# Optimization experiments

Measured on AMD Instinct MI355X. Metric: run time of the kernel, lower is better.

Reference implementation:

```python
import jax, jax.numpy as jnp
import numpy as np

B, S, D, H, F, E = 2, 1024, 1024, 16, 2048, 8
HD = D // H


def _ln(x, g, b, eps=1e-5):
    m = x.mean(-1, keepdims=True)
    v = ((x - m) ** 2).mean(-1, keepdims=True)
    return (x - m) / jnp.sqrt(v + eps) * g + b


def setup_inputs() -> dict:
    key = jax.random.key(0)
    ks = jax.random.split(key, 12)
    rn = lambda k, shp, s=0.02: jax.random.normal(k, shp, jnp.float32) * s
    return {
        'src': jax.random.normal(ks[0], (B, S, D), jnp.float32),
        'q_w': rn(ks[1], (D, D)),
        'k_w': rn(ks[2], (D, D)),
        'v_w': rn(ks[3], (D, D)),
        'out_w': rn(ks[4], (D, D)),
        'gate_w': rn(ks[5], (D, D)),
        'gate_b': rn(ks[6], (D,)),
        'scale_w': rn(ks[7], (H, HD)),
        'n1_g': jnp.ones((D,), jnp.float32),
        'n1_b': jnp.zeros((D,), jnp.float32),
        'n2_g': jnp.ones((D,), jnp.float32),
        'n2_b': jnp.zeros((D,), jnp.float32),
        'moe_gate_w': rn(ks[8], (D, E)),
        'moe_gate_b': jnp.zeros((E,), jnp.float32),
        'w1': rn(ks[9], (E, D, F)),
        'b1': jnp.zeros((E, F), jnp.float32),
        'ln_g': jnp.ones((E, F), jnp.float32),
        'ln_b': jnp.zeros((E, F), jnp.float32),
        'w2': rn(ks[10], (E, F, D)),
        'b2': jnp.zeros((E, D), jnp.float32),
        'res_scale': jnp.ones((E,), jnp.float32),
    }


def reference(src, q_w, k_w, v_w, out_w, gate_w, gate_b, scale_w,
              n1_g, n1_b, n2_g, n2_b, moe_gate_w, moe_gate_b,
              w1, b1, ln_g, ln_b, w2, b2, res_scale):
    b, s, d = src.shape
    h = scale_w.shape[0]
    hd = d // h
    # --- MemoAttention (gated, dynamically scaled), eval mode ---
    q = (src @ q_w).reshape(b, s, h, hd).transpose(0, 2, 1, 3)  # [b,h,s,hd]
    k = (src @ k_w).reshape(b, s, h, hd).transpose(0, 2, 1, 3)
    v = (src @ v_w).reshape(b, s, h, hd).transpose(0, 2, 1, 3)
    scores = jnp.einsum('bhqd,bhkd->bhqk', q, k) / np.float32(np.sqrt(hd))
    scale = jax.nn.sigmoid(jnp.einsum('bhsd,hd->bhs', q, scale_w)) * 2.0
    scores = scores * scale[..., None]
    aw = jax.nn.softmax(scores, axis=-1)
    out = jnp.einsum('bhqk,bhkd->bhqd', aw, v).transpose(0, 2, 1, 3).reshape(b, s, d)
    gate = jax.nn.sigmoid(out @ gate_w + gate_b)
    attn = (out * gate) @ out_w
    # --- residual + norm1 ---
    x = _ln(src + attn, n1_g, n1_b)
    # --- MoE FFN (top-2 routing; torch loop overwrites -> last (max-index) expert
    xr = x.reshape(-1, d)                      # [N, d]
    n = xr.shape[0]
    logits = xr @ moe_gate_w + moe_gate_b       # [N, E]
    top_v, top_i = jax.lax.top_k(logits, 2)
    wts = jax.nn.softmax(top_v, axis=-1)        # [N, 2]
    chosen = jnp.max(top_i, axis=-1)            # last-written expert per token

    def expert(W1, B1, G, Bt, W2, B2, rsc):
        hh = xr @ W1 + B1                       # [N, F]
        hh = jax.nn.gelu(_ln(hh, G, Bt), approximate=False)
        return (hh @ W2 + B2) * rsc + xr        # [N, d]

    outs = jax.vmap(expert)(w1, b1, ln_g, ln_b, w2, b2, res_scale)  # [E,N,d]
    sel = jnp.take_along_axis(outs.transpose(1, 0, 2), chosen[:, None, None], axis=1)[:, 0]
    moe = sel * jnp.sum(wts, axis=-1, keepdims=True)
    # --- residual + norm2 ---
    return _ln(x + moe.reshape(b, s, d), n2_g, n2_b)
```

## Files before the change

### kernel.cpp

```cpp
#include <hip/hip_runtime.h>


typedef _Float16 f16;
typedef _Float16 f16x8 __attribute__((ext_vector_type(8)));
typedef _Float16 f16x4 __attribute__((ext_vector_type(4)));
typedef float f32x4 __attribute__((ext_vector_type(4)));

constexpr int CS  = 1024;
constexpr int CD  = 1024;
constexpr int CH  = 16;
constexpr int CHD = 64;
constexpr int CF  = 2048;
constexpr int CE  = 8;
constexpr int CN  = 2048;
constexpr int CBH = 32;
constexpr int KS  = 512;
constexpr int MAXT = 24;

constexpr float LO_SCALE = 2048.f;
constexpr float LO_INV   = 1.f / 2048.f;

#define MFMA16(a, b, c) __builtin_amdgcn_mfma_f32_16x16x32_f16((a), (b), (c), 0, 0, 0)

#define TO_GBL(p) ((const __attribute__((address_space(1))) void*)(p))
#define TO_LDS(p) ((__attribute__((address_space(3))) void*)(p))
#define GLD16(g, l) __builtin_amdgcn_global_load_lds(TO_GBL(g), TO_LDS(l), 16, 0, 0)

__device__ __forceinline__ void fsplit(float v, f16 &hi, f16 &lo) {
  hi = (f16)v;
  lo = (f16)((v - (float)hi) * LO_SCALE);
}


__global__ void k_split_cvt(const float* __restrict__ in, f16* __restrict__ oh,
                            f16* __restrict__ ol, int n) {
  int i = (blockIdx.x * blockDim.x + threadIdx.x) * 4;
  if (i >= n) return;
  float4 v = *(const float4*)(in + i);
  float a[4] = {v.x, v.y, v.z, v.w};
  f16x4 vh, vl;
#pragma unroll
  for (int j = 0; j < 4; ++j) {
    f16 hi = (f16)a[j];
    vh[j] = hi;
    vl[j] = (f16)((a[j] - (float)hi) * LO_SCALE);
  }
  *(f16x4*)(oh + i) = vh;
  *(f16x4*)(ol + i) = vl;
}

__global__ __launch_bounds__(256) void k_transpose_split(
    const float* __restrict__ in, f16* __restrict__ oh,
    f16* __restrict__ ol, int R, int C) {
  __shared__ float t[64][65];
  const int z = blockIdx.z;
  const float* src = in + (size_t)z * R * C;
  f16* dh = oh + (size_t)z * R * C;
  f16* dl = ol ? ol + (size_t)z * R * C : nullptr;
  const int c0 = blockIdx.x * 64, r0 = blockIdx.y * 64;
  const int tt = threadIdx.x;
  const int lane = tt & 63, wv = tt >> 6;
#pragma unroll
  for (int i = 0; i < 16; ++i)
    t[wv + i * 4][lane] = src[(size_t)(r0 + wv + i * 4) * C + c0 + lane];
  __syncthreads();
  const int oc = tt >> 4;
  const int og = tt & 15;
#pragma unroll
  for (int cc = 0; cc < 64; cc += 16) {
    f16x4 vh, vl;
#pragma unroll
    for (int j = 0; j < 4; ++j) {
      const float v = t[og * 4 + j][cc + oc];
      f16 hi = (f16)v;
      vh[j] = hi;
      vl[j] = (f16)((v - (float)hi) * LO_SCALE);
    }
    const size_t idx = (size_t)(c0 + cc + oc) * R + r0 + og * 4;
    *(f16x4*)(dh + idx) = vh;
    if (dl) *(f16x4*)(dl + idx) = vl;
  }
}


template <bool SPLIT>
__device__ __forceinline__ void gemm_tile128(
    const f16* a0, const f16* a1, const f16* al0, const f16* al1,
    const f16* b0, const f16* b1, const f16* bl0, const f16* bl1,
    int K, f16* lds, f32x4 (&accm)[4][4], f32x4 (&accc)[4][4]) {
  constexpr int BUF = SPLIT ? 16384 : 8192;
  constexpr int BO  = SPLIT ? 8192 : 4096;
  const int t = threadIdx.x;
  const int lane = t & 63, wave = t >> 6;
  const int wm = wave >> 1, wn = wave & 1;
  const int m16 = lane & 15, quad = lane >> 4;
  int aoff[4], boff[4];
#pragma unroll
  for (int s = 0; s < 4; ++s) {
    const int ra = wm * 64 + s * 16 + m16;
    aoff[s] = ra * 32 + ((quad ^ ((ra >> 1) & 3)) * 8);
    const int rb = wn * 64 + s * 16 + m16;
    boff[s] = BO + rb * 32 + ((quad ^ ((rb >> 1) & 3)) * 8);
  }
  auto stage = [&](f16* buf) {
    GLD16(a0, buf + t * 8);
    GLD16(a1, buf + 2048 + t * 8);
    GLD16(b0, buf + BO + t * 8);
    GLD16(b1, buf + BO + 2048 + t * 8);
    if constexpr (SPLIT) {
      GLD16(al0, buf + 4096 + t * 8);
      GLD16(al1, buf + 6144 + t * 8);
      GLD16(bl0, buf + 12288 + t * 8);
      GLD16(bl1, buf + 14336 + t * 8);
      al0 += 32; al1 += 32; bl0 += 32; bl1 += 32;
    }
    a0 += 32; a1 += 32; b0 += 32; b1 += 32;
  };
  stage(lds);
  int cur = 0;
  for (int k = 0; k < K; k += 32) {
    __syncthreads();
    f16* buf = lds + cur * BUF;
    if (k + 32 < K) stage(lds + (cur ^ 1) * BUF);
    f16x8 af[4], alf[4];
#pragma unroll
    for (int s = 0; s < 4; ++s) {
      af[s] = *(const f16x8*)(buf + aoff[s]);
      if constexpr (SPLIT) alf[s] = *(const f16x8*)(buf + 4096 + aoff[s]);
    }
#pragma unroll
    for (int sn = 0; sn < 4; ++sn) {
      const f16x8 bf = *(const f16x8*)(buf + boff[sn]);
#pragma unroll
      for (int sm = 0; sm < 4; ++sm)
        accm[sm][sn] = MFMA16(af[sm], bf, accm[sm][sn]);
      if constexpr (SPLIT) {
        const f16x8 blf = *(const f16x8*)(buf + 4096 + boff[sn]);
#pragma unroll
        for (int sm = 0; sm < 4; ++sm)
          accc[sm][sn] = MFMA16(af[sm], blf, accc[sm][sn]);
#pragma unroll
        for (int sm = 0; sm < 4; ++sm)
          accc[sm][sn] = MFMA16(alf[sm], bf, accc[sm][sn]);
      }
    }
    cur ^= 1;
  }
}


__global__ __launch_bounds__(256, 2) void g_qkv(
    const f16* __restrict__ srcH, const f16* __restrict__ srcL,
    const f16* __restrict__ qwH, const f16* __restrict__ qwL,
    const f16* __restrict__ kwH, const f16* __restrict__ kwL,
    const f16* __restrict__ vwH, const f16* __restrict__ vwL,
    f16* __restrict__ qHo, f16* __restrict__ qLo,
    f16* __restrict__ kHo, f16* __restrict__ kLo,
    f16* __restrict__ vTH, f16* __restrict__ vTL) {
  __shared__ f16 lds[32768];
  const int z = blockIdx.z;
  const int m0 = blockIdx.x * 128, n0 = blockIdx.y * 128;
  const int t = threadIdx.x;
  const int rowS = t >> 2;
  const int ksw = ((t & 3) ^ ((rowS >> 1) & 3)) * 8;
  const f16* BH = (z == 0) ? qwH : (z == 1) ? kwH : vwH;
  const f16* BL = (z == 0) ? qwL : (z == 1) ? kwL : vwL;
  const f16* A0 = srcH + (size_t)(m0 + rowS) * CD + ksw;
  const f16* AL0 = srcL + (size_t)(m0 + rowS) * CD + ksw;
  const f16* B0 = BH + (size_t)(n0 + rowS) * CD + ksw;
  const f16* BL0 = BL + (size_t)(n0 + rowS) * CD + ksw;
  const f32x4 VZ = {0.f, 0.f, 0.f, 0.f};
  f32x4 accm[4][4], accc[4][4];
#pragma unroll
  for (int i = 0; i < 4; ++i)
#pragma unroll
    for (int j = 0; j < 4; ++j) { accm[i][j] = VZ; accc[i][j] = VZ; }
  gemm_tile128<true>(A0, A0 + (size_t)64 * CD, AL0, AL0 + (size_t)64 * CD,
                     B0, B0 + (size_t)64 * CD, BL0, BL0 + (size_t)64 * CD,
                     CD, lds, accm, accc);
  const int lane = t & 63, wave = t >> 6;
  const int wm = wave >> 1, wn = wave & 1;
  const int m16 = lane & 15, quad = lane >> 4;
#pragma unroll
  for (int sm = 0; sm < 4; ++sm)
#pragma unroll
    for (int sn = 0; sn < 4; ++sn)
#pragma unroll
      for (int r = 0; r < 4; ++r) {
        const int row = m0 + wm * 64 + sm * 16 + quad * 4 + r;
        const int col = n0 + wn * 64 + sn * 16 + m16;
        const float v = accm[sm][sn][r] + accc[sm][sn][r] * LO_INV;
        f16 hi, lo; fsplit(v, hi, lo);
        const int bb = row >> 10, ss = row & 1023;
        const int hh = col >> 6, hd = col & 63;
        if (z == 2) {
          const size_t idx = ((size_t)((bb * CH + hh) * CHD + hd)) * CS + ss;
          vTH[idx] = hi; vTL[idx] = lo;
        } else {
          const size_t idx = ((size_t)((bb * CH + hh) * CS + ss)) * CHD + hd;
          if (z == 0) { qHo[idx] = hi; qLo[idx] = lo; }
          else        { kHo[idx] = hi; kLo[idx] = lo; }
        }
      }
}


__device__ __forceinline__ int pswz(int q, int k) {
  return q * 64 + ((((k >> 2) ^ q) & 15) << 2) + (k & 3);
}

__global__ __launch_bounds__(256) void k_fattn(
    const f16* __restrict__ qH_, const f16* __restrict__ qL_,
    const f16* __restrict__ kH_, const f16* __restrict__ kL_,
    const f16* __restrict__ vTH_, const f16* __restrict__ vTL_,
    const float* __restrict__ scale_w,
    f16* __restrict__ aoH, f16* __restrict__ aoL) {
  __shared__ f16 kvb[32768];
  __shared__ float psc[4 * 1024];
  const int bh = blockIdx.y;
  const int b = bh >> 4, h = bh & 15;
  const int t = threadIdx.x;
  const int lane = t & 63, wave = t >> 6;
  const int m16 = lane & 15, quad = lane >> 4;
  const int q0 = blockIdx.x * 64 + wave * 16;
  float* P = psc + wave * 1024;
  const f32x4 VZ = {0.f, 0.f, 0.f, 0.f};
  const size_t kb = (size_t)bh * CS * CHD;

  const int rowS = t >> 3, chS = t & 7;
  auto stage = [&](f16* dst, int kc) {
#pragma unroll
    for (int i = 0; i < 2; ++i) {
      const int row = rowS + 32 * i;
      const int sc = (chS ^ (row & 7)) * 8;
      GLD16(kH_ + kb + (size_t)(kc + row) * CHD + sc, dst + i * 2048 + t * 8);
      GLD16(kL_ + kb + (size_t)(kc + row) * CHD + sc, dst + 4096 + i * 2048 + t * 8);
      GLD16(vTH_ + kb + (size_t)row * CS + kc + sc, dst + 8192 + i * 2048 + t * 8);
      GLD16(vTL_ + kb + (size_t)row * CS + kc + sc, dst + 12288 + i * 2048 + t * 8);
    }
  };
  auto ldf = [&](const f16* piece, int r, int q) -> f16x8 {
    return *(const f16x8*)(piece + r * 64 + ((q ^ (r & 7)) * 8));
  };

  const f16* qrh = qH_ + ((size_t)bh * CS + q0 + m16) * CHD + quad * 8;
  const f16* qrl = qL_ + ((size_t)bh * CS + q0 + m16) * CHD + quad * 8;
  f16x8 a0h = *(const f16x8*)(qrh);
  f16x8 a1h = *(const f16x8*)(qrh + 32);
  f16x8 a0l = *(const f16x8*)(qrl);
  f16x8 a1l = *(const f16x8*)(qrl + 32);

  stage(kvb, 0);

  float dot = 0.f;
  {
    const float* sw = scale_w + h * CHD + quad * 8;
    float4 s0 = *(const float4*)(sw);
    float4 s1 = *(const float4*)(sw + 4);
    float4 s2 = *(const float4*)(sw + 32);
    float4 s3 = *(const float4*)(sw + 36);
    float sv[16] = {s0.x, s0.y, s0.z, s0.w, s1.x, s1.y, s1.z, s1.w,
                    s2.x, s2.y, s2.z, s2.w, s3.x, s3.y, s3.z, s3.w};
#pragma unroll
    for (int j = 0; j < 8; ++j) {
      dot += ((float)a0h[j] + (float)a0l[j] * LO_INV) * sv[j];
      dot += ((float)a1h[j] + (float)a1l[j] * LO_INV) * sv[8 + j];
    }
    dot += __shfl_xor(dot, 16);
    dot += __shfl_xor(dot, 32);
  }
  const float qsv = 2.f / (1.f + __expf(-dot));
  float qsr[4];
#pragma unroll
  for (int r = 0; r < 4; ++r) qsr[r] = __shfl(qsv, quad * 4 + r) * 0.125f;

  f32x4 accm[4], accc[4], accd[4];
#pragma unroll
  for (int tt = 0; tt < 4; ++tt) { accm[tt] = VZ; accc[tt] = VZ; accd[tt] = VZ; }
  float mrun[4], lrun[4];
#pragma unroll
  for (int r = 0; r < 4; ++r) { mrun[r] = -1e30f; lrun[r] = 0.f; }

  int cur = 0;
  for (int kc = 0; kc < CS; kc += 64) {
    __syncthreads();
    const f16* kv = kvb + cur * 16384;
    if (kc + 64 < CS) stage(kvb + (cur ^ 1) * 16384, kc + 64);

    f32x4 st[4];
#pragma unroll
    for (int tt = 0; tt < 4; ++tt) {
      const int r = tt * 16 + m16;
      f16x8 b0h = ldf(kv,        r, quad);
      f16x8 b1h = ldf(kv,        r, quad + 4);
      f16x8 b0l = ldf(kv + 4096, r, quad);
      f16x8 b1l = ldf(kv + 4096, r, quad + 4);
      f32x4 am = VZ, ac1 = VZ, ac2 = VZ;
      am = MFMA16(a0h, b0h, am); am = MFMA16(a1h, b1h, am);
      ac1 = MFMA16(a0h, b0l, ac1); ac2 = MFMA16(a0l, b0h, ac2);
      ac1 = MFMA16(a1h, b1l, ac1); ac2 = MFMA16(a1l, b1h, ac2);
#pragma unroll
      for (int r4 = 0; r4 < 4; ++r4)
        st[tt][r4] = (am[r4] + (ac1[r4] + ac2[r4]) * LO_INV) * qsr[r4];
    }
    float alpha[4];
#pragma unroll
    for (int r = 0; r < 4; ++r) {
      float mx = fmaxf(fmaxf(st[0][r], st[1][r]), fmaxf(st[2][r], st[3][r]));
#pragma unroll
      for (int msk = 8; msk >= 1; msk >>= 1) mx = fmaxf(mx, __shfl_xor(mx, msk));
      const float mnew = fmaxf(mrun[r], mx);
      alpha[r] = __expf(mrun[r] - mnew);
      mrun[r] = mnew;
    }
    float rs[4] = {0.f, 0.f, 0.f, 0.f};
#pragma unroll
    for (int tt = 0; tt < 4; ++tt)
#pragma unroll
      for (int r = 0; r < 4; ++r) {
        const float e = __expf(st[tt][r] - mrun[r]);
        rs[r] += e;
        P[pswz(quad * 4 + r, tt * 16 + m16)] = e;
      }
#pragma unroll
    for (int r = 0; r < 4; ++r) {
#pragma unroll
      for (int msk = 8; msk >= 1; msk >>= 1) rs[r] += __shfl_xor(rs[r], msk);
      lrun[r] = lrun[r] * alpha[r] + rs[r];
#pragma unroll
      for (int tt = 0; tt < 4; ++tt) {
        accm[tt][r] *= alpha[r]; accc[tt][r] *= alpha[r]; accd[tt][r] *= alpha[r];
      }
    }
    f16x8 pah[2], pal[2];
#pragma unroll
    for (int c = 0; c < 2; ++c) {
      const int k0 = c * 32 + quad * 8;
      float4 p0 = *(const float4*)(P + pswz(m16, k0));
      float4 p1 = *(const float4*)(P + pswz(m16, k0 + 4));
      float pv[8] = {p0.x, p0.y, p0.z, p0.w, p1.x, p1.y, p1.z, p1.w};
#pragma unroll
      for (int j = 0; j < 8; ++j) {
        f16 hi = (f16)pv[j];
        pah[c][j] = hi;
        pal[c][j] = (f16)((pv[j] - (float)hi) * LO_SCALE);
      }
    }
#pragma unroll
    for (int c = 0; c < 2; ++c)
#pragma unroll
      for (int tt = 0; tt < 4; ++tt) {
        const int r = tt * 16 + m16;
        f16x8 vbh = ldf(kv + 8192,  r, quad + 4 * c);
        f16x8 vbl = ldf(kv + 12288, r, quad + 4 * c);
        accm[tt] = MFMA16(pah[c], vbh, accm[tt]);
        accc[tt] = MFMA16(pah[c], vbl, accc[tt]);
        accd[tt] = MFMA16(pal[c], vbh, accd[tt]);
      }
    cur ^= 1;
  }
#pragma unroll
  for (int tt = 0; tt < 4; ++tt)
#pragma unroll
    for (int r = 0; r < 4; ++r) {
      const int row = q0 + quad * 4 + r;
      const float v =
          (accm[tt][r] + (accc[tt][r] + accd[tt][r]) * LO_INV) / lrun[r];
      f16 hi, lo; fsplit(v, hi, lo);
      const size_t idx = ((size_t)(b * CS + row)) * CD + h * CHD + tt * 16 + m16;
      aoH[idx] = hi; aoL[idx] = lo;
    }
}


__global__ __launch_bounds__(256, 2) void g_gate(
    const f16* __restrict__ aoH, const f16* __restrict__ aoL,
    const f16* __restrict__ gwH, const f16* __restrict__ gwL,
    float* __restrict__ gpre ) {
  __shared__ f16 lds[32768];
  const int m0 = blockIdx.x * 128, n0 = blockIdx.y * 128, s = blockIdx.z;
  const int t = threadIdx.x;
  const int rowS = t >> 2;
  const int ksw = ((t & 3) ^ ((rowS >> 1) & 3)) * 8;
  const int k0 = s * KS;
  const f16* A0 = aoH + (size_t)(m0 + rowS) * CD + k0 + ksw;
  const f16* AL0 = aoL + (size_t)(m0 + rowS) * CD + k0 + ksw;
  const f16* B0 = gwH + (size_t)(n0 + rowS) * CD + k0 + ksw;
  const f16* BL0 = gwL + (size_t)(n0 + rowS) * CD + k0 + ksw;
  const f32x4 VZ = {0.f, 0.f, 0.f, 0.f};
  f32x4 accm[4][4], accc[4][4];
#pragma unroll
  for (int i = 0; i < 4; ++i)
#pragma unroll
    for (int j = 0; j < 4; ++j) { accm[i][j] = VZ; accc[i][j] = VZ; }
  gemm_tile128<true>(A0, A0 + (size_t)64 * CD, AL0, AL0 + (size_t)64 * CD,
                     B0, B0 + (size_t)64 * CD, BL0, BL0 + (size_t)64 * CD,
                     KS, lds, accm, accc);
  float* gp = gpre + (size_t)s * CN * CD;
  const int lane = t & 63, wave = t >> 6;
  const int wm = wave >> 1, wn = wave & 1;
  const int m16 = lane & 15, quad = lane >> 4;
#pragma unroll
  for (int sm = 0; sm < 4; ++sm)
#pragma unroll
    for (int sn = 0; sn < 4; ++sn)
#pragma unroll
      for (int r = 0; r < 4; ++r) {
        const int row = m0 + wm * 64 + sm * 16 + quad * 4 + r;
        const int col = n0 + wn * 64 + sn * 16 + m16;
        gp[(size_t)row * CD + col] = accm[sm][sn][r] + accc[sm][sn][r] * LO_INV;
      }
}

__global__ __launch_bounds__(256) void k_gatemul(
    const float* __restrict__ gpre, const f16* __restrict__ aoH,
    const f16* __restrict__ aoL, const float* __restrict__ gate_b,
    f16* __restrict__ gdH, f16* __restrict__ gdL) {
  const int i = (blockIdx.x * 256 + threadIdx.x) * 4;
  float4 p0 = *(const float4*)(gpre + i);
  float4 p1 = *(const float4*)(gpre + (size_t)CN * CD + i);
  float4 gb = *(const float4*)(gate_b + (i & (CD - 1)));
  f16x4 ah = *(const f16x4*)(aoH + i);
  f16x4 al = *(const f16x4*)(aoL + i);
  float pre[4] = {p0.x + p1.x + gb.x, p0.y + p1.y + gb.y,
                  p0.z + p1.z + gb.z, p0.w + p1.w + gb.w};
  f16x4 oh, ol;
#pragma unroll
  for (int j = 0; j < 4; ++j) {
    const float g = 1.f / (1.f + __expf(-pre[j]));
    const float ov = ((float)ah[j] + (float)al[j] * LO_INV) * g;
    f16 hi, lo; fsplit(ov, hi, lo);
    oh[j] = hi; ol[j] = lo;
  }
  *(f16x4*)(gdH + i) = oh;
  *(f16x4*)(gdL + i) = ol;
}

__global__ __launch_bounds__(256, 2) void g_outp(
    const f16* __restrict__ gdH, const f16* __restrict__ gdL,
    const f16* __restrict__ owH, const f16* __restrict__ owL,
    float* __restrict__ y1p ) {
  __shared__ f16 lds[32768];
  const int m0 = blockIdx.x * 128, n0 = blockIdx.y * 128, s = blockIdx.z;
  const int t = threadIdx.x;
  const int rowS = t >> 2;
  const int ksw = ((t & 3) ^ ((rowS >> 1) & 3)) * 8;
  const int k0 = s * KS;
  const f16* A0 = gdH + (size_t)(m0 + rowS) * CD + k0 + ksw;
  const f16* AL0 = gdL + (size_t)(m0 + rowS) * CD + k0 + ksw;
  const f16* B0 = owH + (size_t)(n0 + rowS) * CD + k0 + ksw;
  const f16* BL0 = owL + (size_t)(n0 + rowS) * CD + k0 + ksw;
  const f32x4 VZ = {0.f, 0.f, 0.f, 0.f};
  f32x4 accm[4][4], accc[4][4];
#pragma unroll
  for (int i = 0; i < 4; ++i)
#pragma unroll
    for (int j = 0; j < 4; ++j) { accm[i][j] = VZ; accc[i][j] = VZ; }
  gemm_tile128<true>(A0, A0 + (size_t)64 * CD, AL0, AL0 + (size_t)64 * CD,
                     B0, B0 + (size_t)64 * CD, BL0, BL0 + (size_t)64 * CD,
                     KS, lds, accm, accc);
  float* yp = y1p + (size_t)s * CN * CD;
  const int lane = t & 63, wave = t >> 6;
  const int wm = wave >> 1, wn = wave & 1;
  const int m16 = lane & 15, quad = lane >> 4;
#pragma unroll
  for (int sm = 0; sm < 4; ++sm)
#pragma unroll
    for (int sn = 0; sn < 4; ++sn)
#pragma unroll
      for (int r = 0; r < 4; ++r) {
        const int row = m0 + wm * 64 + sm * 16 + quad * 4 + r;
        const int col = n0 + wn * 64 + sn * 16 + m16;
        yp[(size_t)row * CD + col] = accm[sm][sn][r] + accc[sm][sn][r] * LO_INV;
      }
}


__device__ __forceinline__ void block_reduce2(float &s, float &ss, float* red) {
#pragma unroll
  for (int msk = 32; msk >= 1; msk >>= 1) {
    s += __shfl_xor(s, msk);
    ss += __shfl_xor(ss, msk);
  }
  const int wave = threadIdx.x >> 6, lane = threadIdx.x & 63;
  if (lane == 0) { red[wave] = s; red[4 + wave] = ss; }
  __syncthreads();
  s = red[0] + red[1] + red[2] + red[3];
  ss = red[4] + red[5] + red[6] + red[7];
}

__global__ __launch_bounds__(256) void k_ln1(
    const float* __restrict__ y1p, const float* __restrict__ srcp,
    const float* __restrict__ g, const float* __restrict__ bb,
    float* __restrict__ x, f16* __restrict__ xH) {
  __shared__ float red[8];
  const int n = blockIdx.x;
  const int t = threadIdx.x;
  const size_t off = (size_t)n * CD + t * 4;
  float4 v0 = *(const float4*)(y1p + off);
  float4 v1 = *(const float4*)(y1p + (size_t)CN * CD + off);
  float4 v2 = *(const float4*)(srcp + off);
  float a[4] = {v0.x + v1.x + v2.x, v0.y + v1.y + v2.y,
                v0.z + v1.z + v2.z, v0.w + v1.w + v2.w};
  float s = a[0] + a[1] + a[2] + a[3];
  float ss = a[0]*a[0] + a[1]*a[1] + a[2]*a[2] + a[3]*a[3];
  block_reduce2(s, ss, red);
  const float mean = s * (1.f / CD);
  const float var = ss * (1.f / CD) - mean * mean;
  const float rstd = rsqrtf(var + 1e-5f);
#pragma unroll
  for (int j = 0; j < 4; ++j) {
    const int d = t * 4 + j;
    const float val = (a[j] - mean) * rstd * g[d] + bb[d];
    x[(size_t)n * CD + d] = val;
    xH[(size_t)n * CD + d] = (f16)val;
  }
}

__global__ __launch_bounds__(256) void k_ln2(
    const float* __restrict__ zbp, const float* __restrict__ x,
    const float* __restrict__ b2, const float* __restrict__ rsc,
    const int* __restrict__ chosen,
    const float* __restrict__ g, const float* __restrict__ bb,
    float* __restrict__ outp) {
  __shared__ float red[8];
  const int n = blockIdx.x;
  const int e = chosen[n];
  const float rs = rsc[e];
  const int t = threadIdx.x;
  const size_t off = (size_t)n * CD + t * 4;
  float4 p0 = *(const float4*)(zbp + off);
  float4 p1 = *(const float4*)(zbp + (size_t)CN * CD + off);
  float4 p2 = *(const float4*)(zbp + (size_t)2 * CN * CD + off);
  float4 p3 = *(const float4*)(zbp + (size_t)3 * CN * CD + off);
  float4 xv = *(const float4*)(x + off);
  float4 bv = *(const float4*)(b2 + (size_t)e * CD + t * 4);
  float a[4] = {2.f * xv.x + (p0.x + p1.x + p2.x + p3.x + bv.x) * rs,
                2.f * xv.y + (p0.y + p1.y + p2.y + p3.y + bv.y) * rs,
                2.f * xv.z + (p0.z + p1.z + p2.z + p3.z + bv.z) * rs,
                2.f * xv.w + (p0.w + p1.w + p2.w + p3.w + bv.w) * rs};
  float s = a[0] + a[1] + a[2] + a[3];
  float ss = a[0]*a[0] + a[1]*a[1] + a[2]*a[2] + a[3]*a[3];
  block_reduce2(s, ss, red);
  const float mean = s * (1.f / CD);
  const float var = ss * (1.f / CD) - mean * mean;
  const float rstd = rsqrtf(var + 1e-5f);
#pragma unroll
  for (int j = 0; j < 4; ++j) {
    const int d = t * 4 + j;
    outp[(size_t)n * CD + d] = (a[j] - mean) * rstd * g[d] + bb[d];
  }
}


__global__ void k_zero_counts(int* counts) {
  if (threadIdx.x < CE) counts[threadIdx.x] = 0;
}

__global__ __launch_bounds__(256) void k_route(
    const float* __restrict__ x, const float* __restrict__ gw, const float* __restrict__ gb,
    int* __restrict__ chosen, int* __restrict__ counts, int* __restrict__ bucket) {
  const int wave = threadIdx.x >> 6, lane = threadIdx.x & 63;
  const int n = blockIdx.x * 4 + wave;
  const float* xr = x + (size_t)n * CD;
  float acc[CE];
#pragma unroll
  for (int e = 0; e < CE; ++e) acc[e] = 0.f;
  for (int j = 0; j < 16; ++j) {
    const int d = lane * 16 + j;
    const float xv = xr[d];
    const float* wr = gw + (size_t)d * CE;
#pragma unroll
    for (int e = 0; e < CE; ++e) acc[e] += xv * wr[e];
  }
#pragma unroll
  for (int msk = 32; msk >= 1; msk >>= 1) {
#pragma unroll
    for (int e = 0; e < CE; ++e) acc[e] += __shfl_xor(acc[e], msk);
  }
  if (lane == 0) {
    float best = -1e30f, second = -1e30f;
    int bi = 0, si = 0;
#pragma unroll
    for (int e = 0; e < CE; ++e) {
      const float L = acc[e] + gb[e];
      if (L > best) { second = best; si = bi; best = L; bi = e; }
      else if (L > second) { second = L; si = e; }
    }
    const int ch = bi > si ? bi : si;
    chosen[n] = ch;
    const int pos = atomicAdd(&counts[ch], 1);
    bucket[ch * CN + pos] = n;
  }
}

__global__ void k_plan(const int* __restrict__ counts, int* __restrict__ tiles) {
  if (threadIdx.x == 0) {
    int n = 0;
    for (int e = 0; e < CE; ++e) {
      const int c = counts[e];
      for (int m0 = 0; m0 < c; m0 += 128) { tiles[2 * n] = e; tiles[2 * n + 1] = m0; ++n; }
    }
    for (; n < MAXT; ++n) { tiles[2 * n] = -1; tiles[2 * n + 1] = 0; }
  }
}


__global__ __launch_bounds__(256, 2) void g_moe1(
    const f16* __restrict__ xH, const f16* __restrict__ w1t,
    const int* __restrict__ counts, const int* __restrict__ bucket,
    const int* __restrict__ tiles, float* __restrict__ hbp ) {
  const int e = tiles[2 * blockIdx.x];
  if (e < 0) return;
  const int m0 = tiles[2 * blockIdx.x + 1];
  const int cnt = counts[e];
  const int s = blockIdx.z;
  __shared__ f16 lds[16384];
  const int t = threadIdx.x;
  const int rowS = t >> 2;
  const int ksw = ((t & 3) ^ ((rowS >> 1) & 3)) * 8;
  const int k0 = s * KS;
  int ra0 = m0 + rowS;      if (ra0 > cnt - 1) ra0 = cnt - 1;
  int ra1 = m0 + rowS + 64; if (ra1 > cnt - 1) ra1 = cnt - 1;
  const int tok0 = bucket[e * CN + ra0];
  const int tok1 = bucket[e * CN + ra1];
  const int n0 = blockIdx.y * 128;
  const f16* B0 = w1t + ((size_t)e * CF + n0 + rowS) * CD + k0 + ksw;
  const f32x4 VZ = {0.f, 0.f, 0.f, 0.f};
  f32x4 accm[4][4], accd[4][4];
#pragma unroll
  for (int i = 0; i < 4; ++i)
#pragma unroll
    for (int j = 0; j < 4; ++j) { accm[i][j] = VZ; accd[i][j] = VZ; }
  gemm_tile128<false>(xH + (size_t)tok0 * CD + k0 + ksw,
                      xH + (size_t)tok1 * CD + k0 + ksw, nullptr, nullptr,
                      B0, B0 + (size_t)64 * CD, nullptr, nullptr,
                      KS, lds, accm, accd);
  float* hp = hbp + (size_t)s * CN * CF;
  const int lane = t & 63, wave = t >> 6;
  const int wm = wave >> 1, wn = wave & 1;
  const int m16 = lane & 15, quad = lane >> 4;
#pragma unroll
  for (int sm = 0; sm < 4; ++sm)
#pragma unroll
    for (int sn = 0; sn < 4; ++sn)
#pragma unroll
      for (int r = 0; r < 4; ++r) {
        const int rr = m0 + wm * 64 + sm * 16 + quad * 4 + r;
        if (rr >= cnt) continue;
        const int tok = bucket[e * CN + rr];
        const int col = n0 + wn * 64 + sn * 16 + m16;
        hp[(size_t)tok * CF + col] = accm[sm][sn][r];
      }
}

__global__ __launch_bounds__(256) void k_lngelu(
    const float* __restrict__ hbp, const int* __restrict__ chosen,
    const float* __restrict__ b1,
    const float* __restrict__ ln_g, const float* __restrict__ ln_b,
    f16* __restrict__ h2) {
  __shared__ float red[8];
  const int n = blockIdx.x;
  const int e = chosen[n];
  const int t = threadIdx.x;
  const size_t off = (size_t)n * CF + t * 8;
  float4 v0 = *(const float4*)(hbp + off);
  float4 v1 = *(const float4*)(hbp + off + 4);
  float4 u0 = *(const float4*)(hbp + (size_t)CN * CF + off);
  float4 u1 = *(const float4*)(hbp + (size_t)CN * CF + off + 4);
  float4 b0 = *(const float4*)(b1 + (size_t)e * CF + t * 8);
  float4 b1v = *(const float4*)(b1 + (size_t)e * CF + t * 8 + 4);
  float a[8] = {v0.x + u0.x + b0.x, v0.y + u0.y + b0.y,
                v0.z + u0.z + b0.z, v0.w + u0.w + b0.w,
                v1.x + u1.x + b1v.x, v1.y + u1.y + b1v.y,
                v1.z + u1.z + b1v.z, v1.w + u1.w + b1v.w};
  float s = 0.f, ss = 0.f;
#pragma unroll
  for (int j = 0; j < 8; ++j) { s += a[j]; ss += a[j] * a[j]; }
  block_reduce2(s, ss, red);
  const float mean = s * (1.f / CF);
  const float var = ss * (1.f / CF) - mean * mean;
  const float rstd = rsqrtf(var + 1e-5f);
  const float* g = ln_g + (size_t)e * CF;
  const float* bb = ln_b + (size_t)e * CF;
#pragma unroll
  for (int j = 0; j < 8; ++j) {
    const int d = t * 8 + j;
    const float val = (a[j] - mean) * rstd * g[d] + bb[d];
    const float gl = 0.5f * val * (1.f + erff(val * 0.70710678118654752f));
    h2[(size_t)n * CF + d] = (f16)gl;
  }
}

__global__ __launch_bounds__(256, 2) void g_moe2(
    const f16* __restrict__ h2, const f16* __restrict__ w2t,
    const int* __restrict__ counts, const int* __restrict__ bucket,
    const int* __restrict__ tiles, float* __restrict__ zbp ) {
  const int e = tiles[2 * blockIdx.x];
  if (e < 0) return;
  const int m0 = tiles[2 * blockIdx.x + 1];
  const int cnt = counts[e];
  const int s = blockIdx.z;
  __shared__ f16 lds[16384];
  const int t = threadIdx.x;
  const int rowS = t >> 2;
  const int ksw = ((t & 3) ^ ((rowS >> 1) & 3)) * 8;
  const int k0 = s * KS;
  int ra0 = m0 + rowS;      if (ra0 > cnt - 1) ra0 = cnt - 1;
  int ra1 = m0 + rowS + 64; if (ra1 > cnt - 1) ra1 = cnt - 1;
  const int tok0 = bucket[e * CN + ra0];
  const int tok1 = bucket[e * CN + ra1];
  const int n0 = blockIdx.y * 128;
  const f16* B0 = w2t + ((size_t)e * CD + n0 + rowS) * CF + k0 + ksw;
  const f32x4 VZ = {0.f, 0.f, 0.f, 0.f};
  f32x4 accm[4][4], accd[4][4];
#pragma unroll
  for (int i = 0; i < 4; ++i)
#pragma unroll
    for (int j = 0; j < 4; ++j) { accm[i][j] = VZ; accd[i][j] = VZ; }
  gemm_tile128<false>(h2 + (size_t)tok0 * CF + k0 + ksw,
                      h2 + (size_t)tok1 * CF + k0 + ksw, nullptr, nullptr,
                      B0, B0 + (size_t)64 * CF, nullptr, nullptr,
                      KS, lds, accm, accd);
  float* zp = zbp + (size_t)s * CN * CD;
  const int lane = t & 63, wave = t >> 6;
  const int wm = wave >> 1, wn = wave & 1;
  const int m16 = lane & 15, quad = lane >> 4;
#pragma unroll
  for (int sm = 0; sm < 4; ++sm)
#pragma unroll
    for (int sn = 0; sn < 4; ++sn)
#pragma unroll
      for (int r = 0; r < 4; ++r) {
        const int rr = m0 + wm * 64 + sm * 16 + quad * 4 + r;
        if (rr >= cnt) continue;
        const int tok = bucket[e * CN + rr];
        const int col = n0 + wn * 64 + sn * 16 + m16;
        zp[(size_t)tok * CD + col] = accm[sm][sn][r];
      }
}


extern "C" void kernel_launch(void* const* d_in, const int* in_sizes, int n_in,
                              void* d_out, int out_size, void* d_ws, size_t ws_size,
                              hipStream_t stream) {
  (void)in_sizes; (void)n_in; (void)out_size; (void)ws_size;
  const float* src        = (const float*)d_in[0];
  const float* q_w        = (const float*)d_in[1];
  const float* k_w        = (const float*)d_in[2];
  const float* v_w        = (const float*)d_in[3];
  const float* out_w      = (const float*)d_in[4];
  const float* gate_w     = (const float*)d_in[5];
  const float* gate_b     = (const float*)d_in[6];
  const float* scale_w    = (const float*)d_in[7];
  const float* n1_g       = (const float*)d_in[8];
  const float* n1_b       = (const float*)d_in[9];
  const float* n2_g       = (const float*)d_in[10];
  const float* n2_b       = (const float*)d_in[11];
  const float* moe_gate_w = (const float*)d_in[12];
  const float* moe_gate_b = (const float*)d_in[13];
  const float* w1         = (const float*)d_in[14];
  const float* b1         = (const float*)d_in[15];
  const float* ln_g       = (const float*)d_in[16];
  const float* ln_b       = (const float*)d_in[17];
  const float* w2         = (const float*)d_in[18];
  const float* b2         = (const float*)d_in[19];
  const float* res_scale  = (const float*)d_in[20];
  float* outp = (float*)d_out;

  char* p = (char*)d_ws;
  auto take = [&](size_t bytes) -> char* {
    char* r = p;
    p += (bytes + 255) & ~(size_t)255;
    return r;
  };
  f16* srcH = (f16*)take((size_t)CN * CD * 2);
  f16* srcL = (f16*)take((size_t)CN * CD * 2);
  f16* qwH = (f16*)take((size_t)CD * CD * 2);
  f16* qwL = (f16*)take((size_t)CD * CD * 2);
  f16* kwH = (f16*)take((size_t)CD * CD * 2);
  f16* kwL = (f16*)take((size_t)CD * CD * 2);
  f16* vwH = (f16*)take((size_t)CD * CD * 2);
  f16* vwL = (f16*)take((size_t)CD * CD * 2);
  f16* gwH = (f16*)take((size_t)CD * CD * 2);
  f16* gwL = (f16*)take((size_t)CD * CD * 2);
  f16* owH = (f16*)take((size_t)CD * CD * 2);
  f16* owL = (f16*)take((size_t)CD * CD * 2);
  f16* qH = (f16*)take((size_t)CBH * CS * CHD * 2);
  f16* qL = (f16*)take((size_t)CBH * CS * CHD * 2);
  f16* kH = (f16*)take((size_t)CBH * CS * CHD * 2);
  f16* kL = (f16*)take((size_t)CBH * CS * CHD * 2);
  f16* vTH = (f16*)take((size_t)CBH * CS * CHD * 2);
  f16* vTL = (f16*)take((size_t)CBH * CS * CHD * 2);
  f16* aoH = (f16*)take((size_t)CN * CD * 2);
  f16* aoL = (f16*)take((size_t)CN * CD * 2);
  f16* gdH = (f16*)take((size_t)CN * CD * 2);
  f16* gdL = (f16*)take((size_t)CN * CD * 2);
  float* x  = (float*)take((size_t)CN * CD * 4);
  f16* xH = (f16*)take((size_t)CN * CD * 2);
  int* counts = (int*)take(64);
  int* bucket = (int*)take((size_t)CE * CN * 4);
  int* chosen = (int*)take((size_t)CN * 4);
  int* tiles = (int*)take((size_t)MAXT * 2 * 4);
  f16* h2 = (f16*)take((size_t)CN * CF * 2);
  f16* w1t = (f16*)take((size_t)CE * CF * CD * 2);
  f16* w2t = (f16*)take((size_t)CE * CD * CF * 2);
  float* pbuf = (float*)take((size_t)4 * CN * CD * 4);

  k_split_cvt<<<dim3(CN * CD / 4 / 256), 256, 0, stream>>>(src, srcH, srcL, CN * CD);
  k_transpose_split<<<dim3(CD / 64, CD / 64, 1), 256, 0, stream>>>(q_w, qwH, qwL, CD, CD);
  k_transpose_split<<<dim3(CD / 64, CD / 64, 1), 256, 0, stream>>>(k_w, kwH, kwL, CD, CD);
  k_transpose_split<<<dim3(CD / 64, CD / 64, 1), 256, 0, stream>>>(v_w, vwH, vwL, CD, CD);
  k_transpose_split<<<dim3(CD / 64, CD / 64, 1), 256, 0, stream>>>(gate_w, gwH, gwL, CD, CD);
  k_transpose_split<<<dim3(CD / 64, CD / 64, 1), 256, 0, stream>>>(out_w, owH, owL, CD, CD);
  k_transpose_split<<<dim3(CF / 64, CD / 64, CE), 256, 0, stream>>>(w1, w1t, nullptr, CD, CF);
  k_transpose_split<<<dim3(CD / 64, CF / 64, CE), 256, 0, stream>>>(w2, w2t, nullptr, CF, CD);

  g_qkv<<<dim3(CN / 128, CD / 128, 3), 256, 0, stream>>>(
      srcH, srcL, qwH, qwL, kwH, kwL, vwH, vwL, qH, qL, kH, kL, vTH, vTL);
  k_fattn<<<dim3(CS / 64, CBH), 256, 0, stream>>>(
      qH, qL, kH, kL, vTH, vTL, scale_w, aoH, aoL);
  g_gate<<<dim3(CN / 128, CD / 128, 2), 256, 0, stream>>>(aoH, aoL, gwH, gwL, pbuf);
  k_gatemul<<<dim3(CN * CD / 4 / 256), 256, 0, stream>>>(pbuf, aoH, aoL, gate_b, gdH, gdL);
  g_outp<<<dim3(CN / 128, CD / 128, 2), 256, 0, stream>>>(gdH, gdL, owH, owL, pbuf);
  k_ln1<<<dim3(CN), 256, 0, stream>>>(pbuf, src, n1_g, n1_b, x, xH);

  k_zero_counts<<<dim3(1), 64, 0, stream>>>(counts);
  k_route<<<dim3(CN / 4), 256, 0, stream>>>(x, moe_gate_w, moe_gate_b, chosen, counts, bucket);
  k_plan<<<dim3(1), 64, 0, stream>>>(counts, tiles);
  g_moe1<<<dim3(MAXT, CF / 128, 2), 256, 0, stream>>>(xH, w1t, counts, bucket, tiles, pbuf);
  k_lngelu<<<dim3(CN), 256, 0, stream>>>(pbuf, chosen, b1, ln_g, ln_b, h2);
  g_moe2<<<dim3(MAXT, CD / 128, 4), 256, 0, stream>>>(h2, w2t, counts, bucket, tiles, pbuf);
  k_ln2<<<dim3(CN), 256, 0, stream>>>(pbuf, x, b2, res_scale, chosen, n2_g, n2_b, outp);
}
```

Baseline: 515.5 us.

## Vectorize V-transpose stores and streamline flash-attention softmax and block order

The QKV projection epilogue for V now writes four consecutive sequence positions as one f16x4 store, replacing four scalar transposed stores. The attention kernel remaps block IDs to interleave (batch, head) pairs, switches to exp2 with log2e folded into the per-query scale, and skips accumulator rescaling when no row maximum grows. It also merges the two low-order correction accumulators into one, which saves registers but serializes more MFMAs onto a single accumulator chain.

```diff
diff --git a/kernel.cpp b/kernel.cpp
--- a/kernel.cpp
+++ b/kernel.cpp
@@ -181,27 +181,44 @@
   const int lane = t & 63, wave = t >> 6;
   const int wm = wave >> 1, wn = wave & 1;
   const int m16 = lane & 15, quad = lane >> 4;
-#pragma unroll
-  for (int sm = 0; sm < 4; ++sm)
-#pragma unroll
-    for (int sn = 0; sn < 4; ++sn)
-#pragma unroll
-      for (int r = 0; r < 4; ++r) {
-        const int row = m0 + wm * 64 + sm * 16 + quad * 4 + r;
+  if (z == 2) {
+#pragma unroll
+    for (int sm = 0; sm < 4; ++sm)
+#pragma unroll
+      for (int sn = 0; sn < 4; ++sn) {
+        const int row0 = m0 + wm * 64 + sm * 16 + quad * 4;
         const int col = n0 + wn * 64 + sn * 16 + m16;
-        const float v = accm[sm][sn][r] + accc[sm][sn][r] * LO_INV;
-        f16 hi, lo; fsplit(v, hi, lo);
-        const int bb = row >> 10, ss = row & 1023;
+        f16x4 vh, vl;
+#pragma unroll
+        for (int r = 0; r < 4; ++r) {
+          const float v = accm[sm][sn][r] + accc[sm][sn][r] * LO_INV;
+          f16 hi, lo; fsplit(v, hi, lo);
+          vh[r] = hi; vl[r] = lo;
+        }
+        const int bb = row0 >> 10, ss = row0 & 1023;
         const int hh = col >> 6, hd = col & 63;
-        if (z == 2) {
-          const size_t idx = ((size_t)((bb * CH + hh) * CHD + hd)) * CS + ss;
-          vTH[idx] = hi; vTL[idx] = lo;
-        } else {
+        const size_t idx = ((size_t)((bb * CH + hh) * CHD + hd)) * CS + ss;
+        *(f16x4*)(vTH + idx) = vh;
+        *(f16x4*)(vTL + idx) = vl;
+      }
+  } else {
+#pragma unroll
+    for (int sm = 0; sm < 4; ++sm)
+#pragma unroll
+      for (int sn = 0; sn < 4; ++sn)
+#pragma unroll
+        for (int r = 0; r < 4; ++r) {
+          const int row = m0 + wm * 64 + sm * 16 + quad * 4 + r;
+          const int col = n0 + wn * 64 + sn * 16 + m16;
+          const float v = accm[sm][sn][r] + accc[sm][sn][r] * LO_INV;
+          f16 hi, lo; fsplit(v, hi, lo);
+          const int bb = row >> 10, ss = row & 1023;
+          const int hh = col >> 6, hd = col & 63;
           const size_t idx = ((size_t)((bb * CH + hh) * CS + ss)) * CHD + hd;
           if (z == 0) { qHo[idx] = hi; qLo[idx] = lo; }
           else        { kHo[idx] = hi; kLo[idx] = lo; }
         }
-      }
+  }
 }
 
 
@@ -217,12 +234,14 @@
     f16* __restrict__ aoH, f16* __restrict__ aoL) {
   __shared__ f16 kvb[32768];
   __shared__ float psc[4 * 1024];
-  const int bh = blockIdx.y;
+  const int id = blockIdx.x + 16 * blockIdx.y;
+  const int w = (id & 7) * 64 + (id >> 3);
+  const int bh = w >> 4, qc = w & 15;
   const int b = bh >> 4, h = bh & 15;
   const int t = threadIdx.x;
   const int lane = t & 63, wave = t >> 6;
   const int m16 = lane & 15, quad = lane >> 4;
-  const int q0 = blockIdx.x * 64 + wave * 16;
+  const int q0 = qc * 64 + wave * 16;
   float* P = psc + wave * 1024;
   const f32x4 VZ = {0.f, 0.f, 0.f, 0.f};
   const size_t kb = (size_t)bh * CS * CHD;
@@ -252,7 +271,7 @@
 
   stage(kvb, 0);
 
-  float dot = 0.f;
+  float qsr[4];
   {
     const float* sw = scale_w + h * CHD + quad * 8;
     float4 s0 = *(const float4*)(sw);
@@ -261,6 +280,7 @@
     float4 s3 = *(const float4*)(sw + 36);
     float sv[16] = {s0.x, s0.y, s0.z, s0.w, s1.x, s1.y, s1.z, s1.w,
                     s2.x, s2.y, s2.z, s2.w, s3.x, s3.y, s3.z, s3.w};
+    float dot = 0.f;
 #pragma unroll
     for (int j = 0; j < 8; ++j) {
       dot += ((float)a0h[j] + (float)a0l[j] * LO_INV) * sv[j];
@@ -268,15 +288,14 @@
     }
     dot += __shfl_xor(dot, 16);
     dot += __shfl_xor(dot, 32);
-  }
-  const float qsv = 2.f / (1.f + __expf(-dot));
-  float qsr[4];
-#pragma unroll
-  for (int r = 0; r < 4; ++r) qsr[r] = __shfl(qsv, quad * 4 + r) * 0.125f;
-
-  f32x4 accm[4], accc[4], accd[4];
-#pragma unroll
-  for (int tt = 0; tt < 4; ++tt) { accm[tt] = VZ; accc[tt] = VZ; accd[tt] = VZ; }
+    const float qsv = 2.f / (1.f + __expf(-dot)) * (0.125f * 1.44269504f);
+#pragma unroll
+    for (int r = 0; r < 4; ++r) qsr[r] = __shfl(qsv, quad * 4 + r);
+  }
+
+  f32x4 accm[4], accc[4];
+#pragma unroll
+  for (int tt = 0; tt < 4; ++tt) { accm[tt] = VZ; accc[tt] = VZ; }
   float mrun[4], lrun[4];
 #pragma unroll
   for (int r = 0; r < 4; ++r) { mrun[r] = -1e30f; lrun[r] = 0.f; }
@@ -303,22 +322,36 @@
       for (int r4 = 0; r4 < 4; ++r4)
         st[tt][r4] = (am[r4] + (ac1[r4] + ac2[r4]) * LO_INV) * qsr[r4];
     }
-    float alpha[4];
+    float mx[4];
+    bool grow = false;
 #pragma unroll
     for (int r = 0; r < 4; ++r) {
-      float mx = fmaxf(fmaxf(st[0][r], st[1][r]), fmaxf(st[2][r], st[3][r]));
-#pragma unroll
-      for (int msk = 8; msk >= 1; msk >>= 1) mx = fmaxf(mx, __shfl_xor(mx, msk));
-      const float mnew = fmaxf(mrun[r], mx);
-      alpha[r] = __expf(mrun[r] - mnew);
-      mrun[r] = mnew;
+      float m = fmaxf(fmaxf(st[0][r], st[1][r]), fmaxf(st[2][r], st[3][r]));
+#pragma unroll
+      for (int msk = 8; msk >= 1; msk >>= 1) m = fmaxf(m, __shfl_xor(m, msk));
+      mx[r] = m;
+      grow = grow || (m > mrun[r]);
+    }
+    if (__any(grow)) {
+#pragma unroll
+      for (int r = 0; r < 4; ++r) {
+        const float mnew = fmaxf(mrun[r], mx[r]);
+        const float alpha = exp2f(mrun[r] - mnew);
+        mrun[r] = mnew;
+        lrun[r] *= alpha;
+#pragma unroll
+        for (int tt = 0; tt < 4; ++tt) {
+          accm[tt][r] *= alpha;
+          accc[tt][r] *= alpha;
+        }
+      }
     }
     float rs[4] = {0.f, 0.f, 0.f, 0.f};
 #pragma unroll
     for (int tt = 0; tt < 4; ++tt)
 #pragma unroll
       for (int r = 0; r < 4; ++r) {
-        const float e = __expf(st[tt][r] - mrun[r]);
+        const float e = exp2f(st[tt][r] - mrun[r]);
         rs[r] += e;
         P[pswz(quad * 4 + r, tt * 16 + m16)] = e;
       }
@@ -326,11 +359,7 @@
     for (int r = 0; r < 4; ++r) {
 #pragma unroll
       for (int msk = 8; msk >= 1; msk >>= 1) rs[r] += __shfl_xor(rs[r], msk);
-      lrun[r] = lrun[r] * alpha[r] + rs[r];
-#pragma unroll
-      for (int tt = 0; tt < 4; ++tt) {
-        accm[tt][r] *= alpha[r]; accc[tt][r] *= alpha[r]; accd[tt][r] *= alpha[r];
-      }
+      lrun[r] += rs[r];
     }
     f16x8 pah[2], pal[2];
 #pragma unroll
@@ -347,16 +376,20 @@
       }
     }
 #pragma unroll
-    for (int c = 0; c < 2; ++c)
+    for (int c = 0; c < 2; ++c) {
+      f16x8 vbh[4];
 #pragma unroll
       for (int tt = 0; tt < 4; ++tt) {
         const int r = tt * 16 + m16;
-        f16x8 vbh = ldf(kv + 8192,  r, quad + 4 * c);
+        vbh[tt] = ldf(kv + 8192, r, quad + 4 * c);
         f16x8 vbl = ldf(kv + 12288, r, quad + 4 * c);
-        accm[tt] = MFMA16(pah[c], vbh, accm[tt]);
+        accm[tt] = MFMA16(pah[c], vbh[tt], accm[tt]);
         accc[tt] = MFMA16(pah[c], vbl, accc[tt]);
-        accd[tt] = MFMA16(pal[c], vbh, accd[tt]);
-      }
+      }
+#pragma unroll
+      for (int tt = 0; tt < 4; ++tt)
+        accc[tt] = MFMA16(pal[c], vbh[tt], accc[tt]);
+    }
     cur ^= 1;
   }
 #pragma unroll
@@ -364,8 +397,7 @@
 #pragma unroll
     for (int r = 0; r < 4; ++r) {
       const int row = q0 + quad * 4 + r;
-      const float v =
-          (accm[tt][r] + (accc[tt][r] + accd[tt][r]) * LO_INV) / lrun[r];
+      const float v = (accm[tt][r] + accc[tt][r] * LO_INV) / lrun[r];
       f16 hi, lo; fsplit(v, hi, lo);
       const size_t idx = ((size_t)(b * CS + row)) * CD + h * CHD + tt * 16 + m16;
       aoH[idx] = hi; aoL[idx] = lo;
```

After: 522.3 us. No clear change (+1.3%).
